# Optimization experiments

Measured on AMD Instinct MI355X. Metric: run time of the kernel, lower is better.

## Reference

```python
import jax, jax.numpy as jnp
import numpy as np

B, N, DIN = 2, 4096, 128
DQK, DV, H = 128, 128, 8
DH = DQK // H  # head dim for q/k
DVH = DV // H  # head dim for v


def setup_inputs() -> dict:
    key = jax.random.key(0)
    ks = jax.random.split(key, 6)
    x = jax.random.normal(ks[0], (B, N, DIN), dtype=jnp.float32)
    # node mask: first batch fully valid, second batch padded to 3/4 length
    lengths = jnp.array([N, 3 * N // 4])
    mask = jnp.arange(N)[None, :] < lengths[:, None]  # [B, N] bool
    # fused q|k|non_att projection (dim_qk*2 + dim_in outputs)
    W1 = jax.random.normal(ks[1], (DIN, DQK * 2 + DIN), dtype=jnp.float32) * (DIN ** -0.5)
    b1 = jnp.zeros((DQK * 2 + DIN,), dtype=jnp.float32)
    Wv = jax.random.normal(ks[2], (DIN, DV), dtype=jnp.float32) * (DIN ** -0.5)
    bv = jnp.zeros((DV,), dtype=jnp.float32)
    Wo = jax.random.normal(ks[3], (DV, DIN), dtype=jnp.float32) * (DV ** -0.5)
    bo = jnp.zeros((DIN,), dtype=jnp.float32)
    return {"x": x, "mask": mask, "W1": W1, "b1": b1, "Wv": Wv, "bv": bv, "Wo": Wo, "bo": bo}


def reference(x, mask, W1, b1, Wv, bv, Wo, bo):
    # x: [B,N,DIN], mask: [B,N] bool (True = valid node)
    m = mask[..., None].astype(x.dtype)  # [B,N,1]
    # fc_1: fused [q | k | non_att], masked like batch_like(..., skip_masking=False)
    h = (x @ W1 + b1) * m  # [B,N,2*DQK+DIN]
    q = h[..., :DQK]
    k = h[..., DQK:2 * DQK]
    non_att = h[..., -DIN:]
    # fc_v, masked
    v = (x @ Wv + bv) * m  # [B,N,DV]
    # multi-head attention coefficients (AttnCoef(1,1)): masked softmax over keys
    qh = q.reshape(B, N, H, DH)
    kh = k.reshape(B, N, H, DH)
    scores = jnp.einsum('bqhd,bkhd->bhqk', qh, kh) / (DH ** 0.5)  # [B,H,N,N]
    neg = jnp.asarray(jnp.finfo(scores.dtype).min, scores.dtype)
    scores = jnp.where(mask[:, None, None, :], scores, neg)
    alpha = jax.nn.softmax(scores, axis=-1)  # [B,H,N,N]
    # apply_attn: per-head weighted sum of v
    vh = v.reshape(B, N, H, DVH)
    att = jnp.einsum('bhqk,bkhd->bqhd', alpha, vh).reshape(B, N, DV)
    # fc_o (dropout p=0 -> identity), masked; add_batch residual with non_att
    out = (att @ Wo + bo) * m
    return (non_att + out) * m
```

## Files before the change

### kernel.cpp

```cpp
#include <hip/hip_runtime.h>
#include <hip/hip_fp16.h>
#include <math.h>

#define BATCH 2
#define SEQ   4096
#define DIN   128
#define NH    8
#define DHD   16
#define MROWS (BATCH * SEQ)
#define QSCALE 0.36067376022224085f

typedef _Float16 h2 __attribute__((ext_vector_type(2)));
typedef _Float16 h4 __attribute__((ext_vector_type(4)));
typedef _Float16 h8 __attribute__((ext_vector_type(8)));
typedef __fp16   g2 __attribute__((ext_vector_type(2)));
typedef float    f4 __attribute__((ext_vector_type(4)));

__device__ __forceinline__ int keyperm(int k) {
    return ((k >> 5) & 1) * 32 + ((k >> 2) & 3) * 8 + ((k >> 4) & 1) * 4 + (k & 3);
}

__global__ __launch_bounds__(512) void proj_kernel(
    const float* __restrict__ x, const int* __restrict__ mask,
    const float* __restrict__ W1, const float* __restrict__ Wv,
    const float* __restrict__ b1, const float* __restrict__ bv,
    _Float16* __restrict__ qT, _Float16* __restrict__ kT,
    _Float16* __restrict__ vT4, float* __restrict__ nat)
{
    __shared__ __align__(16) char SMEM[128 * 136 * 2];
    _Float16* Tw  = (_Float16*)SMEM;
    _Float16* T16 = (_Float16*)SMEM;
    float*    T32 = (float*)SMEM;

    const int t = threadIdx.x;
    const int w = t >> 6, lane = t & 63, quad = lane >> 4, mr = lane & 15;
    const int region = blockIdx.x;
    const int row0   = blockIdx.y * 128;
    const int col0   = region * 128;

    if (mask[row0] == 0) return;

    h8 a[4];
    {
        const float* xrow = x + (size_t)(row0 + w * 16 + mr) * 128;
#pragma unroll
        for (int ks = 0; ks < 4; ++ks) {
            const float* xs = xrow + ks * 32 + quad * 8;
            float4 x0 = *reinterpret_cast<const float4*>(xs);
            float4 x1 = *reinterpret_cast<const float4*>(xs + 4);
            h8 av;
            av[0] = (_Float16)x0.x; av[1] = (_Float16)x0.y;
            av[2] = (_Float16)x0.z; av[3] = (_Float16)x0.w;
            av[4] = (_Float16)x1.x; av[5] = (_Float16)x1.y;
            av[6] = (_Float16)x1.z; av[7] = (_Float16)x1.w;
            a[ks] = av;
        }
    }

    {
        const float* wsrc = (region < 3) ? (W1 + col0) : Wv;
        const int wstride = (region < 3) ? 384 : 128;
#pragma unroll
        for (int i = 0; i < 8; ++i) {
            int idx = t + i * 512;
            int k = idx >> 5, c4 = idx & 31;
            float4 v = *reinterpret_cast<const float4*>(wsrc + (size_t)k * wstride + c4 * 4);
            Tw[(c4 * 4 + 0) * 136 + k] = (_Float16)v.x;
            Tw[(c4 * 4 + 1) * 136 + k] = (_Float16)v.y;
            Tw[(c4 * 4 + 2) * 136 + k] = (_Float16)v.z;
            Tw[(c4 * 4 + 3) * 136 + k] = (_Float16)v.w;
        }
    }
    __syncthreads();

    f4 acc[8];
#pragma unroll
    for (int ct = 0; ct < 8; ++ct) {
        f4 ac = {0.f, 0.f, 0.f, 0.f};
#pragma unroll
        for (int ks = 0; ks < 4; ++ks) {
            h8 bb = *reinterpret_cast<const h8*>(
                &Tw[(ct * 16 + mr) * 136 + ks * 32 + quad * 8]);
            ac = __builtin_amdgcn_mfma_f32_16x16x32_f16(a[ks], bb, ac, 0, 0, 0);
        }
        acc[ct] = ac;
    }
    __syncthreads();

    if (region <= 1) {
        float scale = (region == 0) ? QSCALE : 1.0f;
#pragma unroll
        for (int ct = 0; ct < 8; ++ct) {
            float bias = b1[col0 + ct * 16 + mr];
#pragma unroll
            for (int reg = 0; reg < 4; ++reg) {
                int lr = w * 16 + quad * 4 + reg;
                T16[lr * 136 + ct * 16 + mr] =
                    (_Float16)((acc[ct][reg] + bias) * scale);
            }
        }
        __syncthreads();
        _Float16* dstbase = (region == 0) ? qT : kT;
#pragma unroll
        for (int i = 0; i < 4; ++i) {
            int idx = t + i * 512;
            int h = idx >> 8, rr = (idx >> 1) & 127, half = idx & 1;
            *reinterpret_cast<h8*>(
                dstbase + ((size_t)h * MROWS + row0 + rr) * 16 + half * 8) =
                *reinterpret_cast<h8*>(&T16[rr * 136 + h * 16 + half * 8]);
        }
    } else if (region == 2) {
#pragma unroll
        for (int p = 0; p < 2; ++p) {
            __syncthreads();
            if ((w >> 2) == p) {
#pragma unroll
                for (int ct = 0; ct < 8; ++ct) {
                    float bias = b1[256 + ct * 16 + mr];
#pragma unroll
                    for (int reg = 0; reg < 4; ++reg) {
                        int lr = (w & 3) * 16 + quad * 4 + reg;
                        T32[lr * 132 + ct * 16 + mr] = acc[ct][reg] + bias;
                    }
                }
            }
            __syncthreads();
#pragma unroll
            for (int i = 0; i < 4; ++i) {
                int idx = t + i * 512;
                int r = idx >> 5, c4 = idx & 31;
                *reinterpret_cast<float4*>(
                    nat + (size_t)(row0 + p * 64 + r) * 128 + c4 * 4) =
                    *reinterpret_cast<float4*>(&T32[r * 132 + c4 * 4]);
            }
        }
    } else {
#pragma unroll
        for (int ct = 0; ct < 8; ++ct) {
            float bias = bv[ct * 16 + mr];
#pragma unroll
            for (int reg = 0; reg < 4; ++reg) {
                int m = w * 16 + quad * 4 + reg;
                int sub = m >> 6, ml = m & 63;
                T16[(ct * 16 + mr) * 136 + sub * 64 + keyperm(ml)] =
                    (_Float16)(acc[ct][reg] + bias);
            }
        }
        __syncthreads();
#pragma unroll
        for (int i = 0; i < 4; ++i) {
            int idx = t + i * 512;
            int c = idx >> 4, sub = (idx >> 3) & 1, seg = idx & 7;
            int h = c >> 4, d = c & 15;
            int tile = blockIdx.y * 2 + sub;
            *reinterpret_cast<h8*>(
                vT4 + ((size_t)(h * 128 + tile) * 16 + d) * 64 + seg * 8) =
                *reinterpret_cast<h8*>(&T16[c * 136 + sub * 64 + seg * 8]);
        }
    }
}

__global__ __launch_bounds__(512) void attn_kernel(
    const _Float16* __restrict__ qT, const _Float16* __restrict__ kT,
    const _Float16* __restrict__ vT4, const int* __restrict__ mask,
    _Float16* __restrict__ att16)
{
    __shared__ float Cmb[4][64][17];

    const int b = blockIdx.z, hh = blockIdx.y, qt = blockIdx.x;
    const int t = threadIdx.x;
    const int w = t >> 6, lane = t & 63, quad = lane >> 4, mr = lane & 15;
    const int wq = w & 3;
    const int g  = w >> 2;
    const int m0 = b * SEQ + qt * 128 + wq * 32;

    if (mask[b * SEQ + qt * 128] == 0) return;

    int tv = mask[b * SEQ + lane * 64];
    const int ntiles = (int)__popcll(__ballot(tv != 0));
    const int half = ntiles >> 1;
    const int n2   = half >> 1;
    const int tA   = g ? half : 0;
    const int tB   = tA + n2;

    h4 aQ[2];
#pragma unroll
    for (int s = 0; s < 2; ++s)
        aQ[s] = *reinterpret_cast<const h4*>(
            qT + ((size_t)hh * MROWS + m0 + s * 16 + mr) * DHD + quad * 4);

    const _Float16* kbase = kT + ((size_t)hh * MROWS + b * SEQ + mr) * DHD + quad * 4;
    const _Float16* vbase = vT4 + ((size_t)(hh * 128 + b * 64) * 16 + mr) * 64 + quad * 8;

    auto ldK = [&](h4* kf, int tile) {
        const _Float16* kp = kbase + (size_t)tile * 1024;
#pragma unroll
        for (int c = 0; c < 4; ++c)
            kf[c] = *reinterpret_cast<const h4*>(kp + c * 16 * DHD);
    };
    auto ldV = [&](h8* vf, int tile) {
        const _Float16* vp = vbase + (size_t)tile * 1024;
#pragma unroll
        for (int kc = 0; kc < 2; ++kc)
            vf[kc] = *reinterpret_cast<const h8*>(vp + kc * 32);
    };

    const _Float16 one = (_Float16)1.0f;
    const h8 vones = {one, one, one, one, one, one, one, one};

    auto proc = [&](h4* kf, h8* vf, f4* O, f4* L) {
#pragma unroll
        for (int s = 0; s < 2; ++s) {
            f4 st[4];
#pragma unroll
            for (int c = 0; c < 4; ++c)
                st[c] = __builtin_amdgcn_mfma_f32_16x16x16f16(
                    kf[c], aQ[s], (f4){0.f, 0.f, 0.f, 0.f}, 0, 0, 0);

            h8 aP[2];
#pragma unroll
            for (int kc = 0; kc < 2; ++kc) {
                h8 p;
#pragma unroll
                for (int hf = 0; hf < 2; ++hf) {
                    int c = 2 * kc + hf;
                    g2 s01 = __builtin_amdgcn_cvt_pkrtz(st[c][0], st[c][1]);
                    g2 s23 = __builtin_amdgcn_cvt_pkrtz(st[c][2], st[c][3]);
                    __half2 e01 = h2exp2(*reinterpret_cast<__half2*>(&s01));
                    __half2 e23 = h2exp2(*reinterpret_cast<__half2*>(&s23));
                    h2 p01 = *reinterpret_cast<h2*>(&e01);
                    h2 p23 = *reinterpret_cast<h2*>(&e23);
                    p[hf * 4 + 0] = p01[0]; p[hf * 4 + 1] = p01[1];
                    p[hf * 4 + 2] = p23[0]; p[hf * 4 + 3] = p23[1];
                }
                aP[kc] = p;
            }
#pragma unroll
            for (int kc = 0; kc < 2; ++kc) {
                O[s] = __builtin_amdgcn_mfma_f32_16x16x32_f16(aP[kc], vf[kc], O[s], 0, 0, 0);
                L[s] = __builtin_amdgcn_mfma_f32_16x16x32_f16(aP[kc], vones,  L[s], 0, 0, 0);
            }
        }
    };

    h4 kA[4], kB[4]; h8 vA[2], vB[2];
    ldK(kA, tA); ldV(vA, tA);
    ldK(kB, tB); ldV(vB, tB);

    f4 OA[2] = {{0.f,0.f,0.f,0.f},{0.f,0.f,0.f,0.f}};
    f4 OB[2] = {{0.f,0.f,0.f,0.f},{0.f,0.f,0.f,0.f}};
    f4 LA[2] = {{0.f,0.f,0.f,0.f},{0.f,0.f,0.f,0.f}};
    f4 LB[2] = {{0.f,0.f,0.f,0.f},{0.f,0.f,0.f,0.f}};

    for (int i = 0; i < n2; ++i) {
        proc(kA, vA, OA, LA);
        int nA = (i + 1 < n2) ? (tA + i + 1) : (tA + i);
        ldK(kA, nA); ldV(vA, nA);

        proc(kB, vB, OB, LB);
        int nB = (i + 1 < n2) ? (tB + i + 1) : (tB + i);
        ldK(kB, nB); ldV(vB, nB);
    }

    f4 O[2], accL[2];
#pragma unroll
    for (int s = 0; s < 2; ++s) {
        O[s]    = OA[s] + OB[s];
        accL[s] = LA[s] + LB[s];
    }

    if (g == 1) {
#pragma unroll
        for (int s = 0; s < 2; ++s)
#pragma unroll
            for (int reg = 0; reg < 4; ++reg) {
                Cmb[wq][lane][s * 4 + reg]     = O[s][reg];
                Cmb[wq][lane][8 + s * 4 + reg] = accL[s][reg];
            }
    }
    __syncthreads();
    if (g == 0) {
#pragma unroll
        for (int s = 0; s < 2; ++s)
#pragma unroll
            for (int reg = 0; reg < 4; ++reg) {
                float of = O[s][reg]    + Cmb[wq][lane][s * 4 + reg];
                float lf = accL[s][reg] + Cmb[wq][lane][8 + s * 4 + reg];
                att16[(size_t)(m0 + s * 16 + quad * 4 + reg) * 128 + hh * DHD + mr] =
                    (_Float16)(of / lf);
            }
    }
}

__global__ __launch_bounds__(256) void outproj_kernel(
    const _Float16* __restrict__ att16, const float* __restrict__ Wo,
    const float* __restrict__ nat, const int* __restrict__ mask,
    const float* __restrict__ bo, float* __restrict__ out)
{
    __shared__ __align__(16) _Float16 Tw[64 * 136];

    const int t = threadIdx.x;
    const int w = t >> 6, lane = t & 63, quad = lane >> 4, mr = lane & 15;
    const int row0 = blockIdx.x * 64;
    const int m0 = row0 + w * 16;
    const int c0 = blockIdx.y * 64;

    if (mask[row0] == 0) {
#pragma unroll
        for (int i = 0; i < 4; ++i) {
            int idx = t + i * 256;
            int r = idx >> 4, c4 = idx & 15;
            *reinterpret_cast<float4*>(
                out + (size_t)(row0 + r) * 128 + c0 + c4 * 4) =
                (float4){0.f, 0.f, 0.f, 0.f};
        }
        return;
    }

#pragma unroll
    for (int i = 0; i < 8; ++i) {
        int idx = t + i * 256;
        int k = idx >> 4, c4 = idx & 15;
        float4 v = *reinterpret_cast<const float4*>(Wo + (size_t)k * 128 + c0 + c4 * 4);
        Tw[(c4 * 4 + 0) * 136 + k] = (_Float16)v.x;
        Tw[(c4 * 4 + 1) * 136 + k] = (_Float16)v.y;
        Tw[(c4 * 4 + 2) * 136 + k] = (_Float16)v.z;
        Tw[(c4 * 4 + 3) * 136 + k] = (_Float16)v.w;
    }
    __syncthreads();

    h8 a[4];
#pragma unroll
    for (int ks = 0; ks < 4; ++ks)
        a[ks] = *reinterpret_cast<const h8*>(
            att16 + (size_t)(m0 + mr) * 128 + ks * 32 + quad * 8);

    f4 acc[4];
#pragma unroll
    for (int ct = 0; ct < 4; ++ct) {
        f4 ac = {0.f, 0.f, 0.f, 0.f};
#pragma unroll
        for (int ks = 0; ks < 4; ++ks) {
            h8 bb = *reinterpret_cast<const h8*>(
                &Tw[(ct * 16 + mr) * 136 + ks * 32 + quad * 8]);
            ac = __builtin_amdgcn_mfma_f32_16x16x32_f16(a[ks], bb, ac, 0, 0, 0);
        }
        acc[ct] = ac;
    }

#pragma unroll
    for (int ct = 0; ct < 4; ++ct) {
        float bias = bo[c0 + ct * 16 + mr];
#pragma unroll
        for (int reg = 0; reg < 4; ++reg) {
            int row = m0 + quad * 4 + reg;
            int col = c0 + ct * 16 + mr;
            out[(size_t)row * 128 + col] =
                acc[ct][reg] + bias + nat[(size_t)row * 128 + col];
        }
    }
}

extern "C" void kernel_launch(void* const* d_in, const int* in_sizes, int n_in,
                              void* d_out, int out_size, void* d_ws, size_t ws_size,
                              hipStream_t stream) {
    const float* x    = (const float*)d_in[0];
    const int*   mask = (const int*)  d_in[1];
    const float* W1   = (const float*)d_in[2];
    const float* b1   = (const float*)d_in[3];
    const float* Wv   = (const float*)d_in[4];
    const float* bv   = (const float*)d_in[5];
    const float* Wo   = (const float*)d_in[6];
    const float* bo   = (const float*)d_in[7];
    float* out = (float*)d_out;

    _Float16* qT    = (_Float16*)d_ws;
    _Float16* kT    = qT    + (size_t)NH * MROWS * DHD;
    _Float16* vT4   = kT    + (size_t)NH * MROWS * DHD;
    _Float16* att16 = vT4   + (size_t)DIN * MROWS;
    float*    nat   = (float*)(att16 + (size_t)MROWS * DIN);

    proj_kernel<<<dim3(4, MROWS / 128), 512, 0, stream>>>(
        x, mask, W1, Wv, b1, bv, qT, kT, vT4, nat);
    attn_kernel<<<dim3(SEQ / 128, NH, BATCH), 512, 0, stream>>>(
        qT, kT, vT4, mask, att16);
    outproj_kernel<<<dim3(MROWS / 64, 2), 256, 0, stream>>>(
        att16, Wo, nat, mask, bo, out);
}
```

Baseline: 129.0 us.

## Fuse projection, attention and output projection into one cooperative persistent kernel

Merges the three kernels into one kernel launched cooperatively with 256 blocks, separating the projection, attention and output-projection phases with grid-wide syncs. Each block takes two half-width projection tasks and two attention tasks, and the output projection is repartitioned across 8 waves per block. The goal is to drop the launch gaps between kernels. In exchange it adds grid barrier cost and fixes parallelism at 256 blocks, which may leave CUs idle or unbalanced when masked tiles are skipped.

```diff
diff --git a/kernel.cpp b/kernel.cpp
--- a/kernel.cpp
+++ b/kernel.cpp
@@ -1,6 +1,9 @@
 #include <hip/hip_runtime.h>
 #include <hip/hip_fp16.h>
+#include <hip/hip_cooperative_groups.h>
 #include <math.h>
+
+namespace cg = cooperative_groups;
 
 #define BATCH 2
 #define SEQ   4096
@@ -20,343 +23,346 @@
     return ((k >> 5) & 1) * 32 + ((k >> 2) & 3) * 8 + ((k >> 4) & 1) * 4 + (k & 3);
 }
 
-__global__ __launch_bounds__(512) void proj_kernel(
+__global__ __launch_bounds__(512) void fused_kernel(
     const float* __restrict__ x, const int* __restrict__ mask,
     const float* __restrict__ W1, const float* __restrict__ Wv,
     const float* __restrict__ b1, const float* __restrict__ bv,
+    const float* __restrict__ Wo, const float* __restrict__ bo,
     _Float16* __restrict__ qT, _Float16* __restrict__ kT,
-    _Float16* __restrict__ vT4, float* __restrict__ nat)
+    _Float16* __restrict__ vT4, _Float16* __restrict__ att16,
+    float* __restrict__ nat, float* __restrict__ out)
 {
-    __shared__ __align__(16) char SMEM[128 * 136 * 2];
-    _Float16* Tw  = (_Float16*)SMEM;
-    _Float16* T16 = (_Float16*)SMEM;
-    float*    T32 = (float*)SMEM;
-
+    __shared__ __align__(16) char SMEM[34816];
+    _Float16* Tw   = (_Float16*)SMEM;
+    _Float16* T16  = (_Float16*)SMEM;
+    _Float16* T16v = (_Float16*)SMEM;
+    float*    T32  = (float*)SMEM;
+
+    const int bid = blockIdx.x;
     const int t = threadIdx.x;
     const int w = t >> 6, lane = t & 63, quad = lane >> 4, mr = lane & 15;
-    const int region = blockIdx.x;
-    const int row0   = blockIdx.y * 128;
-    const int col0   = region * 128;
-
-    if (mask[row0] == 0) return;
-
-    h8 a[4];
-    {
-        const float* xrow = x + (size_t)(row0 + w * 16 + mr) * 128;
-#pragma unroll
-        for (int ks = 0; ks < 4; ++ks) {
-            const float* xs = xrow + ks * 32 + quad * 8;
-            float4 x0 = *reinterpret_cast<const float4*>(xs);
-            float4 x1 = *reinterpret_cast<const float4*>(xs + 4);
-            h8 av;
-            av[0] = (_Float16)x0.x; av[1] = (_Float16)x0.y;
-            av[2] = (_Float16)x0.z; av[3] = (_Float16)x0.w;
-            av[4] = (_Float16)x1.x; av[5] = (_Float16)x1.y;
-            av[6] = (_Float16)x1.z; av[7] = (_Float16)x1.w;
-            a[ks] = av;
+
+    cg::grid_group grid = cg::this_grid();
+
+    for (int rep = 0; rep < 2; ++rep) {
+        int task = bid * 2 + rep;
+        int region = task >> 7;
+        int ch     = (task >> 6) & 1;
+        int rowt   = task & 63;
+        int row0   = rowt * 128;
+        int col0   = region * 128 + ch * 64;
+        bool act   = (mask[row0] != 0);
+
+        __syncthreads();
+        if (act) {
+            h8 a[4];
+            {
+                const float* xrow = x + (size_t)(row0 + w * 16 + mr) * 128;
+#pragma unroll
+                for (int ks = 0; ks < 4; ++ks) {
+                    const float* xs = xrow + ks * 32 + quad * 8;
+                    float4 x0 = *reinterpret_cast<const float4*>(xs);
+                    float4 x1 = *reinterpret_cast<const float4*>(xs + 4);
+                    h8 av;
+                    av[0] = (_Float16)x0.x; av[1] = (_Float16)x0.y;
+                    av[2] = (_Float16)x0.z; av[3] = (_Float16)x0.w;
+                    av[4] = (_Float16)x1.x; av[5] = (_Float16)x1.y;
+                    av[6] = (_Float16)x1.z; av[7] = (_Float16)x1.w;
+                    a[ks] = av;
+                }
+            }
+            {
+                const float* wsrc = (region < 3) ? (W1 + col0) : (Wv + ch * 64);
+                const int wstride = (region < 3) ? 384 : 128;
+#pragma unroll
+                for (int i = 0; i < 4; ++i) {
+                    int idx = t + i * 512;
+                    int k = idx >> 4, c4 = idx & 15;
+                    float4 v = *reinterpret_cast<const float4*>(
+                        wsrc + (size_t)k * wstride + c4 * 4);
+                    Tw[(c4 * 4 + 0) * 136 + k] = (_Float16)v.x;
+                    Tw[(c4 * 4 + 1) * 136 + k] = (_Float16)v.y;
+                    Tw[(c4 * 4 + 2) * 136 + k] = (_Float16)v.z;
+                    Tw[(c4 * 4 + 3) * 136 + k] = (_Float16)v.w;
+                }
+            }
+            __syncthreads();
+
+            f4 acc[4];
+#pragma unroll
+            for (int ct = 0; ct < 4; ++ct) {
+                f4 ac = {0.f, 0.f, 0.f, 0.f};
+#pragma unroll
+                for (int ks = 0; ks < 4; ++ks) {
+                    h8 bb = *reinterpret_cast<const h8*>(
+                        &Tw[(ct * 16 + mr) * 136 + ks * 32 + quad * 8]);
+                    ac = __builtin_amdgcn_mfma_f32_16x16x32_f16(a[ks], bb, ac, 0, 0, 0);
+                }
+                acc[ct] = ac;
+            }
+            __syncthreads();
+
+            if (region <= 1) {
+                float scale = (region == 0) ? QSCALE : 1.0f;
+#pragma unroll
+                for (int ct = 0; ct < 4; ++ct) {
+                    float bias = b1[col0 + ct * 16 + mr];
+#pragma unroll
+                    for (int reg = 0; reg < 4; ++reg) {
+                        int lr = w * 16 + quad * 4 + reg;
+                        T16[lr * 80 + ct * 16 + mr] =
+                            (_Float16)((acc[ct][reg] + bias) * scale);
+                    }
+                }
+                __syncthreads();
+                _Float16* dstbase = (region == 0) ? qT : kT;
+#pragma unroll
+                for (int i = 0; i < 2; ++i) {
+                    int idx = t + i * 512;
+                    int hloc = idx >> 8, rr = (idx >> 1) & 127, half = idx & 1;
+                    *reinterpret_cast<h8*>(
+                        dstbase + ((size_t)(ch * 4 + hloc) * MROWS + row0 + rr) * 16 + half * 8) =
+                        *reinterpret_cast<h8*>(&T16[rr * 80 + hloc * 16 + half * 8]);
+                }
+            } else if (region == 2) {
+#pragma unroll
+                for (int ct = 0; ct < 4; ++ct) {
+                    float bias = b1[col0 + ct * 16 + mr];
+#pragma unroll
+                    for (int reg = 0; reg < 4; ++reg) {
+                        int lr = w * 16 + quad * 4 + reg;
+                        T32[lr * 68 + ct * 16 + mr] = acc[ct][reg] + bias;
+                    }
+                }
+                __syncthreads();
+#pragma unroll
+                for (int i = 0; i < 4; ++i) {
+                    int idx = t + i * 512;
+                    int r = idx >> 4, c4 = idx & 15;
+                    *reinterpret_cast<float4*>(
+                        nat + (size_t)(row0 + r) * 128 + ch * 64 + c4 * 4) =
+                        *reinterpret_cast<float4*>(&T32[r * 68 + c4 * 4]);
+                }
+            } else {
+#pragma unroll
+                for (int ct = 0; ct < 4; ++ct) {
+                    float bias = bv[ch * 64 + ct * 16 + mr];
+#pragma unroll
+                    for (int reg = 0; reg < 4; ++reg) {
+                        int m = w * 16 + quad * 4 + reg;
+                        int sub = m >> 6, ml = m & 63;
+                        T16v[(ct * 16 + mr) * 136 + sub * 64 + keyperm(ml)] =
+                            (_Float16)(acc[ct][reg] + bias);
+                    }
+                }
+                __syncthreads();
+#pragma unroll
+                for (int i = 0; i < 2; ++i) {
+                    int idx = t + i * 512;
+                    int c = idx >> 4, sub = (idx >> 3) & 1, seg = idx & 7;
+                    int h = ch * 4 + (c >> 4), d = c & 15;
+                    int tile = rowt * 2 + sub;
+                    *reinterpret_cast<h8*>(
+                        vT4 + ((size_t)(h * 128 + tile) * 16 + d) * 64 + seg * 8) =
+                        *reinterpret_cast<h8*>(&T16v[c * 136 + sub * 64 + seg * 8]);
+                }
+            }
         }
     }
 
+    grid.sync();
+
     {
-        const float* wsrc = (region < 3) ? (W1 + col0) : Wv;
-        const int wstride = (region < 3) ? 384 : 128;
-#pragma unroll
-        for (int i = 0; i < 8; ++i) {
-            int idx = t + i * 512;
-            int k = idx >> 5, c4 = idx & 31;
-            float4 v = *reinterpret_cast<const float4*>(wsrc + (size_t)k * wstride + c4 * 4);
-            Tw[(c4 * 4 + 0) * 136 + k] = (_Float16)v.x;
-            Tw[(c4 * 4 + 1) * 136 + k] = (_Float16)v.y;
-            Tw[(c4 * 4 + 2) * 136 + k] = (_Float16)v.z;
-            Tw[(c4 * 4 + 3) * 136 + k] = (_Float16)v.w;
+        float (*Cmb)[64][17] = (float(*)[64][17])SMEM;
+        const int wq = w & 3;
+        const int g  = w >> 2;
+
+        for (int rep = 0; rep < 2; ++rep) {
+            int task = bid * 2 + rep;
+            int qt = task & 31, hh = (task >> 5) & 7, b = task >> 8;
+            int m0 = b * SEQ + qt * 128 + wq * 32;
+            bool act = (mask[b * SEQ + qt * 128] != 0);
+
+            f4 O[2], accL[2];
+            if (act) {
+                int tv = mask[b * SEQ + lane * 64];
+                const int ntiles = (int)__popcll(__ballot(tv != 0));
+                const int half = ntiles >> 1;
+                const int n2   = half >> 1;
+                const int tA   = g ? half : 0;
+                const int tB   = tA + n2;
+
+                h4 aQ[2];
+#pragma unroll
+                for (int s = 0; s < 2; ++s)
+                    aQ[s] = *reinterpret_cast<const h4*>(
+                        qT + ((size_t)hh * MROWS + m0 + s * 16 + mr) * DHD + quad * 4);
+
+                const _Float16* kbase = kT + ((size_t)hh * MROWS + b * SEQ + mr) * DHD + quad * 4;
+                const _Float16* vbase = vT4 + ((size_t)(hh * 128 + b * 64) * 16 + mr) * 64 + quad * 8;
+
+                auto ldK = [&](h4* kf, int tile) {
+                    const _Float16* kp = kbase + (size_t)tile * 1024;
+#pragma unroll
+                    for (int c = 0; c < 4; ++c)
+                        kf[c] = *reinterpret_cast<const h4*>(kp + c * 16 * DHD);
+                };
+                auto ldV = [&](h8* vf, int tile) {
+                    const _Float16* vp = vbase + (size_t)tile * 1024;
+#pragma unroll
+                    for (int kc = 0; kc < 2; ++kc)
+                        vf[kc] = *reinterpret_cast<const h8*>(vp + kc * 32);
+                };
+
+                const _Float16 one = (_Float16)1.0f;
+                const h8 vones = {one, one, one, one, one, one, one, one};
+
+                auto proc = [&](h4* kf, h8* vf, f4* Op, f4* Lp) {
+#pragma unroll
+                    for (int s = 0; s < 2; ++s) {
+                        f4 st[4];
+#pragma unroll
+                        for (int c = 0; c < 4; ++c)
+                            st[c] = __builtin_amdgcn_mfma_f32_16x16x16f16(
+                                kf[c], aQ[s], (f4){0.f, 0.f, 0.f, 0.f}, 0, 0, 0);
+                        h8 aP[2];
+#pragma unroll
+                        for (int kc = 0; kc < 2; ++kc) {
+                            h8 p;
+#pragma unroll
+                            for (int hf = 0; hf < 2; ++hf) {
+                                int c = 2 * kc + hf;
+                                g2 s01 = __builtin_amdgcn_cvt_pkrtz(st[c][0], st[c][1]);
+                                g2 s23 = __builtin_amdgcn_cvt_pkrtz(st[c][2], st[c][3]);
+                                __half2 e01 = h2exp2(*reinterpret_cast<__half2*>(&s01));
+                                __half2 e23 = h2exp2(*reinterpret_cast<__half2*>(&s23));
+                                h2 p01 = *reinterpret_cast<h2*>(&e01);
+                                h2 p23 = *reinterpret_cast<h2*>(&e23);
+                                p[hf * 4 + 0] = p01[0]; p[hf * 4 + 1] = p01[1];
+                                p[hf * 4 + 2] = p23[0]; p[hf * 4 + 3] = p23[1];
+                            }
+                            aP[kc] = p;
+                        }
+#pragma unroll
+                        for (int kc = 0; kc < 2; ++kc) {
+                            Op[s] = __builtin_amdgcn_mfma_f32_16x16x32_f16(aP[kc], vf[kc], Op[s], 0, 0, 0);
+                            Lp[s] = __builtin_amdgcn_mfma_f32_16x16x32_f16(aP[kc], vones,  Lp[s], 0, 0, 0);
+                        }
+                    }
+                };
+
+                h4 kA[4], kB[4]; h8 vA[2], vB[2];
+                ldK(kA, tA); ldV(vA, tA);
+                ldK(kB, tB); ldV(vB, tB);
+
+                f4 OA[2] = {{0.f,0.f,0.f,0.f},{0.f,0.f,0.f,0.f}};
+                f4 OB[2] = {{0.f,0.f,0.f,0.f},{0.f,0.f,0.f,0.f}};
+                f4 LA[2] = {{0.f,0.f,0.f,0.f},{0.f,0.f,0.f,0.f}};
+                f4 LB[2] = {{0.f,0.f,0.f,0.f},{0.f,0.f,0.f,0.f}};
+
+                for (int i = 0; i < n2; ++i) {
+                    proc(kA, vA, OA, LA);
+                    int nA = (i + 1 < n2) ? (tA + i + 1) : (tA + i);
+                    ldK(kA, nA); ldV(vA, nA);
+                    proc(kB, vB, OB, LB);
+                    int nB = (i + 1 < n2) ? (tB + i + 1) : (tB + i);
+                    ldK(kB, nB); ldV(vB, nB);
+                }
+#pragma unroll
+                for (int s = 0; s < 2; ++s) {
+                    O[s]    = OA[s] + OB[s];
+                    accL[s] = LA[s] + LB[s];
+                }
+            }
+
+            __syncthreads();
+            if (act && g == 1) {
+#pragma unroll
+                for (int s = 0; s < 2; ++s)
+#pragma unroll
+                    for (int reg = 0; reg < 4; ++reg) {
+                        Cmb[wq][lane][s * 4 + reg]     = O[s][reg];
+                        Cmb[wq][lane][8 + s * 4 + reg] = accL[s][reg];
+                    }
+            }
+            __syncthreads();
+            if (act && g == 0) {
+#pragma unroll
+                for (int s = 0; s < 2; ++s)
+#pragma unroll
+                    for (int reg = 0; reg < 4; ++reg) {
+                        float of = O[s][reg]    + Cmb[wq][lane][s * 4 + reg];
+                        float lf = accL[s][reg] + Cmb[wq][lane][8 + s * 4 + reg];
+                        att16[(size_t)(m0 + s * 16 + quad * 4 + reg) * 128 + hh * DHD + mr] =
+                            (_Float16)(of / lf);
+                    }
+            }
         }
     }
-    __syncthreads();
-
-    f4 acc[8];
-#pragma unroll
-    for (int ct = 0; ct < 8; ++ct) {
-        f4 ac = {0.f, 0.f, 0.f, 0.f};
-#pragma unroll
-        for (int ks = 0; ks < 4; ++ks) {
-            h8 bb = *reinterpret_cast<const h8*>(
-                &Tw[(ct * 16 + mr) * 136 + ks * 32 + quad * 8]);
-            ac = __builtin_amdgcn_mfma_f32_16x16x32_f16(a[ks], bb, ac, 0, 0, 0);
-        }
-        acc[ct] = ac;
-    }
-    __syncthreads();
-
-    if (region <= 1) {
-        float scale = (region == 0) ? QSCALE : 1.0f;
-#pragma unroll
-        for (int ct = 0; ct < 8; ++ct) {
-            float bias = b1[col0 + ct * 16 + mr];
-#pragma unroll
-            for (int reg = 0; reg < 4; ++reg) {
-                int lr = w * 16 + quad * 4 + reg;
-                T16[lr * 136 + ct * 16 + mr] =
-                    (_Float16)((acc[ct][reg] + bias) * scale);
-            }
-        }
+
+    grid.sync();
+
+    {
+        int task = bid;
+        int rowt = task >> 1, chb = task & 1;
+        int row0 = rowt * 64;
+        int c0   = chb * 64;
+        const int rw = w >> 1, cw = w & 1;
+        const int m0w = row0 + rw * 16;
+
         __syncthreads();
-        _Float16* dstbase = (region == 0) ? qT : kT;
-#pragma unroll
-        for (int i = 0; i < 4; ++i) {
-            int idx = t + i * 512;
-            int h = idx >> 8, rr = (idx >> 1) & 127, half = idx & 1;
-            *reinterpret_cast<h8*>(
-                dstbase + ((size_t)h * MROWS + row0 + rr) * 16 + half * 8) =
-                *reinterpret_cast<h8*>(&T16[rr * 136 + h * 16 + half * 8]);
-        }
-    } else if (region == 2) {
-#pragma unroll
-        for (int p = 0; p < 2; ++p) {
-            __syncthreads();
-            if ((w >> 2) == p) {
-#pragma unroll
-                for (int ct = 0; ct < 8; ++ct) {
-                    float bias = b1[256 + ct * 16 + mr];
-#pragma unroll
-                    for (int reg = 0; reg < 4; ++reg) {
-                        int lr = (w & 3) * 16 + quad * 4 + reg;
-                        T32[lr * 132 + ct * 16 + mr] = acc[ct][reg] + bias;
-                    }
-                }
-            }
-            __syncthreads();
+        if (mask[row0] == 0) {
+#pragma unroll
+            for (int i = 0; i < 2; ++i) {
+                int idx = t + i * 512;
+                int r = idx >> 4, c4 = idx & 15;
+                *reinterpret_cast<float4*>(
+                    out + (size_t)(row0 + r) * 128 + c0 + c4 * 4) =
+                    (float4){0.f, 0.f, 0.f, 0.f};
+            }
+        } else {
 #pragma unroll
             for (int i = 0; i < 4; ++i) {
                 int idx = t + i * 512;
-                int r = idx >> 5, c4 = idx & 31;
-                *reinterpret_cast<float4*>(
-                    nat + (size_t)(row0 + p * 64 + r) * 128 + c4 * 4) =
-                    *reinterpret_cast<float4*>(&T32[r * 132 + c4 * 4]);
-            }
-        }
-    } else {
-#pragma unroll
-        for (int ct = 0; ct < 8; ++ct) {
-            float bias = bv[ct * 16 + mr];
-#pragma unroll
-            for (int reg = 0; reg < 4; ++reg) {
-                int m = w * 16 + quad * 4 + reg;
-                int sub = m >> 6, ml = m & 63;
-                T16[(ct * 16 + mr) * 136 + sub * 64 + keyperm(ml)] =
-                    (_Float16)(acc[ct][reg] + bias);
-            }
-        }
-        __syncthreads();
-#pragma unroll
-        for (int i = 0; i < 4; ++i) {
-            int idx = t + i * 512;
-            int c = idx >> 4, sub = (idx >> 3) & 1, seg = idx & 7;
-            int h = c >> 4, d = c & 15;
-            int tile = blockIdx.y * 2 + sub;
-            *reinterpret_cast<h8*>(
-                vT4 + ((size_t)(h * 128 + tile) * 16 + d) * 64 + seg * 8) =
-                *reinterpret_cast<h8*>(&T16[c * 136 + sub * 64 + seg * 8]);
-        }
-    }
-}
-
-__global__ __launch_bounds__(512) void attn_kernel(
-    const _Float16* __restrict__ qT, const _Float16* __restrict__ kT,
-    const _Float16* __restrict__ vT4, const int* __restrict__ mask,
-    _Float16* __restrict__ att16)
-{
-    __shared__ float Cmb[4][64][17];
-
-    const int b = blockIdx.z, hh = blockIdx.y, qt = blockIdx.x;
-    const int t = threadIdx.x;
-    const int w = t >> 6, lane = t & 63, quad = lane >> 4, mr = lane & 15;
-    const int wq = w & 3;
-    const int g  = w >> 2;
-    const int m0 = b * SEQ + qt * 128 + wq * 32;
-
-    if (mask[b * SEQ + qt * 128] == 0) return;
-
-    int tv = mask[b * SEQ + lane * 64];
-    const int ntiles = (int)__popcll(__ballot(tv != 0));
-    const int half = ntiles >> 1;
-    const int n2   = half >> 1;
-    const int tA   = g ? half : 0;
-    const int tB   = tA + n2;
-
-    h4 aQ[2];
-#pragma unroll
-    for (int s = 0; s < 2; ++s)
-        aQ[s] = *reinterpret_cast<const h4*>(
-            qT + ((size_t)hh * MROWS + m0 + s * 16 + mr) * DHD + quad * 4);
-
-    const _Float16* kbase = kT + ((size_t)hh * MROWS + b * SEQ + mr) * DHD + quad * 4;
-    const _Float16* vbase = vT4 + ((size_t)(hh * 128 + b * 64) * 16 + mr) * 64 + quad * 8;
-
-    auto ldK = [&](h4* kf, int tile) {
-        const _Float16* kp = kbase + (size_t)tile * 1024;
-#pragma unroll
-        for (int c = 0; c < 4; ++c)
-            kf[c] = *reinterpret_cast<const h4*>(kp + c * 16 * DHD);
-    };
-    auto ldV = [&](h8* vf, int tile) {
-        const _Float16* vp = vbase + (size_t)tile * 1024;
-#pragma unroll
-        for (int kc = 0; kc < 2; ++kc)
-            vf[kc] = *reinterpret_cast<const h8*>(vp + kc * 32);
-    };
-
-    const _Float16 one = (_Float16)1.0f;
-    const h8 vones = {one, one, one, one, one, one, one, one};
-
-    auto proc = [&](h4* kf, h8* vf, f4* O, f4* L) {
-#pragma unroll
-        for (int s = 0; s < 2; ++s) {
-            f4 st[4];
-#pragma unroll
-            for (int c = 0; c < 4; ++c)
-                st[c] = __builtin_amdgcn_mfma_f32_16x16x16f16(
-                    kf[c], aQ[s], (f4){0.f, 0.f, 0.f, 0.f}, 0, 0, 0);
-
-            h8 aP[2];
-#pragma unroll
-            for (int kc = 0; kc < 2; ++kc) {
-                h8 p;
-#pragma unroll
-                for (int hf = 0; hf < 2; ++hf) {
-                    int c = 2 * kc + hf;
-                    g2 s01 = __builtin_amdgcn_cvt_pkrtz(st[c][0], st[c][1]);
-                    g2 s23 = __builtin_amdgcn_cvt_pkrtz(st[c][2], st[c][3]);
-                    __half2 e01 = h2exp2(*reinterpret_cast<__half2*>(&s01));
-                    __half2 e23 = h2exp2(*reinterpret_cast<__half2*>(&s23));
-                    h2 p01 = *reinterpret_cast<h2*>(&e01);
-                    h2 p23 = *reinterpret_cast<h2*>(&e23);
-                    p[hf * 4 + 0] = p01[0]; p[hf * 4 + 1] = p01[1];
-                    p[hf * 4 + 2] = p23[0]; p[hf * 4 + 3] = p23[1];
-                }
-                aP[kc] = p;
-            }
-#pragma unroll
-            for (int kc = 0; kc < 2; ++kc) {
-                O[s] = __builtin_amdgcn_mfma_f32_16x16x32_f16(aP[kc], vf[kc], O[s], 0, 0, 0);
-                L[s] = __builtin_amdgcn_mfma_f32_16x16x32_f16(aP[kc], vones,  L[s], 0, 0, 0);
-            }
-        }
-    };
-
-    h4 kA[4], kB[4]; h8 vA[2], vB[2];
-    ldK(kA, tA); ldV(vA, tA);
-    ldK(kB, tB); ldV(vB, tB);
-
-    f4 OA[2] = {{0.f,0.f,0.f,0.f},{0.f,0.f,0.f,0.f}};
-    f4 OB[2] = {{0.f,0.f,0.f,0.f},{0.f,0.f,0.f,0.f}};
-    f4 LA[2] = {{0.f,0.f,0.f,0.f},{0.f,0.f,0.f,0.f}};
-    f4 LB[2] = {{0.f,0.f,0.f,0.f},{0.f,0.f,0.f,0.f}};
-
-    for (int i = 0; i < n2; ++i) {
-        proc(kA, vA, OA, LA);
-        int nA = (i + 1 < n2) ? (tA + i + 1) : (tA + i);
-        ldK(kA, nA); ldV(vA, nA);
-
-        proc(kB, vB, OB, LB);
-        int nB = (i + 1 < n2) ? (tB + i + 1) : (tB + i);
-        ldK(kB, nB); ldV(vB, nB);
-    }
-
-    f4 O[2], accL[2];
-#pragma unroll
-    for (int s = 0; s < 2; ++s) {
-        O[s]    = OA[s] + OB[s];
-        accL[s] = LA[s] + LB[s];
-    }
-
-    if (g == 1) {
-#pragma unroll
-        for (int s = 0; s < 2; ++s)
-#pragma unroll
-            for (int reg = 0; reg < 4; ++reg) {
-                Cmb[wq][lane][s * 4 + reg]     = O[s][reg];
-                Cmb[wq][lane][8 + s * 4 + reg] = accL[s][reg];
-            }
-    }
-    __syncthreads();
-    if (g == 0) {
-#pragma unroll
-        for (int s = 0; s < 2; ++s)
-#pragma unroll
-            for (int reg = 0; reg < 4; ++reg) {
-                float of = O[s][reg]    + Cmb[wq][lane][s * 4 + reg];
-                float lf = accL[s][reg] + Cmb[wq][lane][8 + s * 4 + reg];
-                att16[(size_t)(m0 + s * 16 + quad * 4 + reg) * 128 + hh * DHD + mr] =
-                    (_Float16)(of / lf);
-            }
-    }
-}
-
-__global__ __launch_bounds__(256) void outproj_kernel(
-    const _Float16* __restrict__ att16, const float* __restrict__ Wo,
-    const float* __restrict__ nat, const int* __restrict__ mask,
-    const float* __restrict__ bo, float* __restrict__ out)
-{
-    __shared__ __align__(16) _Float16 Tw[64 * 136];
-
-    const int t = threadIdx.x;
-    const int w = t >> 6, lane = t & 63, quad = lane >> 4, mr = lane & 15;
-    const int row0 = blockIdx.x * 64;
-    const int m0 = row0 + w * 16;
-    const int c0 = blockIdx.y * 64;
-
-    if (mask[row0] == 0) {
-#pragma unroll
-        for (int i = 0; i < 4; ++i) {
-            int idx = t + i * 256;
-            int r = idx >> 4, c4 = idx & 15;
-            *reinterpret_cast<float4*>(
-                out + (size_t)(row0 + r) * 128 + c0 + c4 * 4) =
-                (float4){0.f, 0.f, 0.f, 0.f};
-        }
-        return;
-    }
-
-#pragma unroll
-    for (int i = 0; i < 8; ++i) {
-        int idx = t + i * 256;
-        int k = idx >> 4, c4 = idx & 15;
-        float4 v = *reinterpret_cast<const float4*>(Wo + (size_t)k * 128 + c0 + c4 * 4);
-        Tw[(c4 * 4 + 0) * 136 + k] = (_Float16)v.x;
-        Tw[(c4 * 4 + 1) * 136 + k] = (_Float16)v.y;
-        Tw[(c4 * 4 + 2) * 136 + k] = (_Float16)v.z;
-        Tw[(c4 * 4 + 3) * 136 + k] = (_Float16)v.w;
-    }
-    __syncthreads();
-
-    h8 a[4];
-#pragma unroll
-    for (int ks = 0; ks < 4; ++ks)
-        a[ks] = *reinterpret_cast<const h8*>(
-            att16 + (size_t)(m0 + mr) * 128 + ks * 32 + quad * 8);
-
-    f4 acc[4];
-#pragma unroll
-    for (int ct = 0; ct < 4; ++ct) {
-        f4 ac = {0.f, 0.f, 0.f, 0.f};
-#pragma unroll
-        for (int ks = 0; ks < 4; ++ks) {
-            h8 bb = *reinterpret_cast<const h8*>(
-                &Tw[(ct * 16 + mr) * 136 + ks * 32 + quad * 8]);
-            ac = __builtin_amdgcn_mfma_f32_16x16x32_f16(a[ks], bb, ac, 0, 0, 0);
-        }
-        acc[ct] = ac;
-    }
-
-#pragma unroll
-    for (int ct = 0; ct < 4; ++ct) {
-        float bias = bo[c0 + ct * 16 + mr];
-#pragma unroll
-        for (int reg = 0; reg < 4; ++reg) {
-            int row = m0 + quad * 4 + reg;
-            int col = c0 + ct * 16 + mr;
-            out[(size_t)row * 128 + col] =
-                acc[ct][reg] + bias + nat[(size_t)row * 128 + col];
+                int k = idx >> 4, c4 = idx & 15;
+                float4 v = *reinterpret_cast<const float4*>(
+                    Wo + (size_t)k * 128 + c0 + c4 * 4);
+                Tw[(c4 * 4 + 0) * 136 + k] = (_Float16)v.x;
+                Tw[(c4 * 4 + 1) * 136 + k] = (_Float16)v.y;
+                Tw[(c4 * 4 + 2) * 136 + k] = (_Float16)v.z;
+                Tw[(c4 * 4 + 3) * 136 + k] = (_Float16)v.w;
+            }
+            __syncthreads();
+
+            h8 a[4];
+#pragma unroll
+            for (int ks = 0; ks < 4; ++ks)
+                a[ks] = *reinterpret_cast<const h8*>(
+                    att16 + (size_t)(m0w + mr) * 128 + ks * 32 + quad * 8);
+
+            f4 acc[2];
+#pragma unroll
+            for (int ct = 0; ct < 2; ++ct) {
+                f4 ac = {0.f, 0.f, 0.f, 0.f};
+#pragma unroll
+                for (int ks = 0; ks < 4; ++ks) {
+                    h8 bb = *reinterpret_cast<const h8*>(
+                        &Tw[(cw * 32 + ct * 16 + mr) * 136 + ks * 32 + quad * 8]);
+                    ac = __builtin_amdgcn_mfma_f32_16x16x32_f16(a[ks], bb, ac, 0, 0, 0);
+                }
+                acc[ct] = ac;
+            }
+#pragma unroll
+            for (int ct = 0; ct < 2; ++ct) {
+                int col = c0 + cw * 32 + ct * 16 + mr;
+                float bias = bo[col];
+#pragma unroll
+                for (int reg = 0; reg < 4; ++reg) {
+                    int row = m0w + quad * 4 + reg;
+                    out[(size_t)row * 128 + col] =
+                        acc[ct][reg] + bias + nat[(size_t)row * 128 + col];
+                }
+            }
         }
     }
 }
@@ -380,10 +386,11 @@
     _Float16* att16 = vT4   + (size_t)DIN * MROWS;
     float*    nat   = (float*)(att16 + (size_t)MROWS * DIN);
 
-    proj_kernel<<<dim3(4, MROWS / 128), 512, 0, stream>>>(
-        x, mask, W1, Wv, b1, bv, qT, kT, vT4, nat);
-    attn_kernel<<<dim3(SEQ / 128, NH, BATCH), 512, 0, stream>>>(
-        qT, kT, vT4, mask, att16);
-    outproj_kernel<<<dim3(MROWS / 64, 2), 256, 0, stream>>>(
-        att16, Wo, nat, mask, bo, out);
+    void* args[] = {
+        (void*)&x, (void*)&mask, (void*)&W1, (void*)&Wv, (void*)&b1,
+        (void*)&bv, (void*)&Wo, (void*)&bo, (void*)&qT, (void*)&kT,
+        (void*)&vT4, (void*)&att16, (void*)&nat, (void*)&out
+    };
+    hipLaunchCooperativeKernel((const void*)fused_kernel, dim3(256), dim3(512),
+                               args, 0, stream);
 }
```

After: 210.1 us. +62.9%, slower.
